# Kernel optimization log

Hardware: AMD Instinct MI355X
Metric: run time of the kernel (lower is better)

## Reference

```python
import jax, jax.numpy as jnp
import numpy as np

NUM_HEADS = 32
NUM_KV_HEADS = 8
HEAD_DIM = 128
ATTN_SCALE = 0.08838834764831845  # 1/sqrt(128)
CONTEXT_LEN = 8192
BLOCK_SIZE = 16
NUM_BLOCKS = 1024  # physical blocks -> 16384 cache slots


def setup_inputs() -> dict:
    key = jax.random.key(0)
    ks = jax.random.split(key, 6)
    q = jax.random.normal(ks[0], (1, NUM_HEADS, HEAD_DIM), jnp.float32)
    k = jax.random.normal(ks[1], (1, NUM_KV_HEADS, HEAD_DIM), jnp.float32)
    v = jax.random.normal(ks[2], (1, NUM_KV_HEADS, HEAD_DIM), jnp.float32)
    num_slots = NUM_BLOCKS * BLOCK_SIZE
    k_cache = jax.random.normal(ks[3], (num_slots, NUM_KV_HEADS, HEAD_DIM), jnp.float32)
    v_cache = jax.random.normal(ks[4], (num_slots, NUM_KV_HEADS, HEAD_DIM), jnp.float32)
    num_logical = CONTEXT_LEN // BLOCK_SIZE
    block_table = jax.random.permutation(ks[5], NUM_BLOCKS)[:num_logical].astype(jnp.int32)
    # new token is written at logical position context_len - 1
    last = CONTEXT_LEN - 1
    slot_mapping = (block_table[last // BLOCK_SIZE] * BLOCK_SIZE + last % BLOCK_SIZE)[None].astype(jnp.int32)
    return {"q": q, "k": k, "v": v, "k_cache": k_cache, "v_cache": v_cache,
            "block_table": block_table, "slot_mapping": slot_mapping,
            "context_len": CONTEXT_LEN, "block_size": BLOCK_SIZE}


def reference(q, k, v, k_cache, v_cache, block_table, slot_mapping, context_len, block_size):
    # _write_to_cache: scatter the new token's K/V into the paged cache
    k_cache = k_cache.at[slot_mapping].set(k)
    v_cache = v_cache.at[slot_mapping].set(v)
    # _build_full_slot_mapping + _read_from_cache: gather full context K/V
    pos = jnp.arange(context_len)
    slots = block_table[pos // block_size] * block_size + pos % block_size  # (S,)
    k_all = k_cache[slots]  # (S, Hkv, D)
    v_all = v_cache[slots]
    # GQA: repeat_interleave KV heads to match query heads
    g = NUM_HEADS // NUM_KV_HEADS
    k_all = jnp.repeat(k_all, g, axis=1)  # (S, H, D)
    v_all = jnp.repeat(v_all, g, axis=1)
    # manual masked SDPA; num_query_tokens == 1 -> mask is all-ones (no tril)
    scores = jnp.einsum('qhd,khd->hqk', q, k_all) * ATTN_SCALE  # (H, 1, S)
    weights = jax.nn.softmax(scores, axis=-1)
    out = jnp.einsum('hqk,khd->qhd', weights, v_all)  # (1, H, D)
    return out
```

## Files before the change

kernel.cpp:

```cpp
#include <hip/hip_runtime.h>
#include <math.h>


#define NUM_HEADS    32
#define NUM_KV_HEADS 8
#define GQA          4
#define HEAD_DIM     128
#define ATTN_SCALE   0.08838834764831845f
#define CTX          8192
#define BLK          16
#define SPLITS       64
#define CHUNK        (CTX / SPLITS)
#define POS_PER_WAVE (CHUNK / 4)
#define ITERS        (POS_PER_WAVE / 2)

__global__ __launch_bounds__(256) void attn_partial(
    const float* __restrict__ q,
    const float* __restrict__ knew,
    const float* __restrict__ vnew,
    const float* __restrict__ kc,
    const float* __restrict__ vc,
    const int*   __restrict__ bt,
    float*       __restrict__ o_part,
    float2*      __restrict__ ml_part)
{
    const int split = blockIdx.x;
    const int kvh   = blockIdx.y;
    const int tid   = threadIdx.x;
    const int wave  = tid >> 6;
    const int lane  = tid & 63;
    const int half  = lane >> 5;
    const int l     = lane & 31;

    float4 qf[GQA];
#pragma unroll
    for (int h = 0; h < GQA; ++h)
        qf[h] = *(const float4*)(q + (kvh * GQA + h) * HEAD_DIM + l * 4);

    float  m[GQA], lsum[GQA];
    float4 o[GQA];
#pragma unroll
    for (int h = 0; h < GQA; ++h) {
        m[h] = -INFINITY; lsum[h] = 0.f;
        o[h] = make_float4(0.f, 0.f, 0.f, 0.f);
    }

    const int base = split * CHUNK + wave * POS_PER_WAVE;

    for (int it = 0; it < ITERS; ++it) {
        const int pos  = base + it * 2 + half;
        const int slot = bt[pos >> 4] * BLK + (pos & 15);

        const float* kptr;
        const float* vptr;
        if (pos == CTX - 1) {
            kptr = knew + kvh * HEAD_DIM;
            vptr = vnew + kvh * HEAD_DIM;
        } else {
            const size_t row = ((size_t)slot * NUM_KV_HEADS + kvh) * HEAD_DIM;
            kptr = kc + row;
            vptr = vc + row;
        }
        const float4 kf = *(const float4*)(kptr + l * 4);
        const float4 vf = *(const float4*)(vptr + l * 4);

        float s[GQA];
#pragma unroll
        for (int h = 0; h < GQA; ++h)
            s[h] = qf[h].x * kf.x + qf[h].y * kf.y + qf[h].z * kf.z + qf[h].w * kf.w;

#pragma unroll
        for (int off = 16; off >= 1; off >>= 1) {
#pragma unroll
            for (int h = 0; h < GQA; ++h)
                s[h] += __shfl_xor(s[h], off, 64);
        }

#pragma unroll
        for (int h = 0; h < GQA; ++h) {
            const float sc    = s[h] * ATTN_SCALE;
            const float mn    = fmaxf(m[h], sc);
            const float alpha = __expf(m[h] - mn);
            const float p     = __expf(sc - mn);
            m[h] = mn;
            lsum[h] = lsum[h] * alpha + p;
            o[h].x = o[h].x * alpha + p * vf.x;
            o[h].y = o[h].y * alpha + p * vf.y;
            o[h].z = o[h].z * alpha + p * vf.z;
            o[h].w = o[h].w * alpha + p * vf.w;
        }
    }

    __shared__ float lds_o[8][GQA][HEAD_DIM];
    __shared__ float lds_m[8][GQA];
    __shared__ float lds_l[8][GQA];

    const int halfid = tid >> 5;
#pragma unroll
    for (int h = 0; h < GQA; ++h) {
        *(float4*)&lds_o[halfid][h][l * 4] = o[h];
        if (l == 0) { lds_m[halfid][h] = m[h]; lds_l[halfid][h] = lsum[h]; }
    }
    __syncthreads();

    if (tid < HEAD_DIM) {
        const int d = tid;
#pragma unroll
        for (int h = 0; h < GQA; ++h) {
            float M = -INFINITY;
#pragma unroll
            for (int i = 0; i < 8; ++i) M = fmaxf(M, lds_m[i][h]);
            float acc = 0.f, L = 0.f;
#pragma unroll
            for (int i = 0; i < 8; ++i) {
                const float w = __expf(lds_m[i][h] - M);
                L   += w * lds_l[i][h];
                acc += w * lds_o[i][h][d];
            }
            const int head = kvh * GQA + h;
            o_part[((size_t)head * SPLITS + split) * HEAD_DIM + d] = acc;
            if (d == 0) ml_part[head * SPLITS + split] = make_float2(M, L);
        }
    }
}

__global__ __launch_bounds__(128) void attn_reduce(
    const float*  __restrict__ o_part,
    const float2* __restrict__ ml_part,
    float*        __restrict__ out)
{
    const int h = blockIdx.x;
    const int d = threadIdx.x;

    __shared__ float2 mls[SPLITS];
    if (d < SPLITS) mls[d] = ml_part[h * SPLITS + d];
    __syncthreads();

    float M = -INFINITY;
#pragma unroll 8
    for (int s = 0; s < SPLITS; ++s) M = fmaxf(M, mls[s].x);

    float acc = 0.f, L = 0.f;
#pragma unroll 4
    for (int s = 0; s < SPLITS; ++s) {
        const float w = __expf(mls[s].x - M);
        L   += w * mls[s].y;
        acc += w * o_part[((size_t)h * SPLITS + s) * HEAD_DIM + d];
    }
    out[h * HEAD_DIM + d] = acc / L;
}

extern "C" void kernel_launch(void* const* d_in, const int* in_sizes, int n_in,
                              void* d_out, int out_size, void* d_ws, size_t ws_size,
                              hipStream_t stream) {
    const float* q    = (const float*)d_in[0];
    const float* knew = (const float*)d_in[1];
    const float* vnew = (const float*)d_in[2];
    const float* kc   = (const float*)d_in[3];
    const float* vc   = (const float*)d_in[4];
    const int*   bt   = (const int*)d_in[5];

    float*  o_part  = (float*)d_ws;
    float2* ml_part = (float2*)((char*)d_ws + (size_t)NUM_HEADS * SPLITS * HEAD_DIM * sizeof(float));

    attn_partial<<<dim3(SPLITS, NUM_KV_HEADS), 256, 0, stream>>>(
        q, knew, vnew, kc, vc, bt, o_part, ml_part);
    attn_reduce<<<NUM_HEADS, HEAD_DIM, 0, stream>>>(o_part, ml_part, (float*)d_out);
}
```

Baseline: 173.4 us.

## Raise split count and batch all KV loads per thread before compute

Raises the number of context splits from 64 to 256, so each block covers 32 positions (two cache blocks) and each half-wave handles 4 positions. All K/V loads for those positions are issued up front into registers, and the two block-table entries are loaded once per block instead of once per position. The goal is more memory-level parallelism and more blocks in flight for this bandwidth-bound decode attention. In exchange, the reduce kernel has to combine 4x more partials and the partial-output workspace traffic grows.

Result: no change. 174.6 us (+0.7%).

```diff
diff --git a/kernel.cpp b/kernel.cpp
--- a/kernel.cpp
+++ b/kernel.cpp
@@ -9,12 +9,11 @@
 #define ATTN_SCALE   0.08838834764831845f
 #define CTX          8192
 #define BLK          16
-#define SPLITS       64
+#define SPLITS       256
 #define CHUNK        (CTX / SPLITS)
-#define POS_PER_WAVE (CHUNK / 4)
-#define ITERS        (POS_PER_WAVE / 2)
+#define PPH          4
 
-__global__ __launch_bounds__(256) void attn_partial(
+__global__ __launch_bounds__(256, 4) void attn_partial(
     const float* __restrict__ q,
     const float* __restrict__ knew,
     const float* __restrict__ vnew,
@@ -32,25 +31,22 @@
     const int half  = lane >> 5;
     const int l     = lane & 31;
 
+    const int bt0 = bt[split * 2];
+    const int bt1 = bt[split * 2 + 1];
+
     float4 qf[GQA];
 #pragma unroll
     for (int h = 0; h < GQA; ++h)
         qf[h] = *(const float4*)(q + (kvh * GQA + h) * HEAD_DIM + l * 4);
 
-    float  m[GQA], lsum[GQA];
-    float4 o[GQA];
+    const int pbase = wave * (2 * PPH) + half;
+    float4 kf[PPH], vf[PPH];
 #pragma unroll
-    for (int h = 0; h < GQA; ++h) {
-        m[h] = -INFINITY; lsum[h] = 0.f;
-        o[h] = make_float4(0.f, 0.f, 0.f, 0.f);
-    }
-
-    const int base = split * CHUNK + wave * POS_PER_WAVE;
-
-    for (int it = 0; it < ITERS; ++it) {
-        const int pos  = base + it * 2 + half;
-        const int slot = bt[pos >> 4] * BLK + (pos & 15);
-
+    for (int it = 0; it < PPH; ++it) {
+        const int off = pbase + it * 2;
+        const int pos = split * CHUNK + off;
+        const int blk = (off >> 4) ? bt1 : bt0;
+        const int slot = blk * BLK + (pos & 15);
         const float* kptr;
         const float* vptr;
         if (pos == CTX - 1) {
@@ -61,33 +57,47 @@
             kptr = kc + row;
             vptr = vc + row;
         }
-        const float4 kf = *(const float4*)(kptr + l * 4);
-        const float4 vf = *(const float4*)(vptr + l * 4);
+        kf[it] = *(const float4*)(kptr + l * 4);
+        vf[it] = *(const float4*)(vptr + l * 4);
+    }
 
-        float s[GQA];
+    float s[PPH][GQA];
+#pragma unroll
+    for (int it = 0; it < PPH; ++it)
 #pragma unroll
         for (int h = 0; h < GQA; ++h)
-            s[h] = qf[h].x * kf.x + qf[h].y * kf.y + qf[h].z * kf.z + qf[h].w * kf.w;
+            s[it][h] = qf[h].x * kf[it].x + qf[h].y * kf[it].y +
+                       qf[h].z * kf[it].z + qf[h].w * kf[it].w;
 
 #pragma unroll
-        for (int off = 16; off >= 1; off >>= 1) {
+    for (int off = 16; off >= 1; off >>= 1)
+#pragma unroll
+        for (int it = 0; it < PPH; ++it)
 #pragma unroll
             for (int h = 0; h < GQA; ++h)
-                s[h] += __shfl_xor(s[h], off, 64);
-        }
+                s[it][h] += __shfl_xor(s[it][h], off, 64);
 
+    float  m[GQA], lsum[GQA];
+    float4 o[GQA];
+#pragma unroll
+    for (int h = 0; h < GQA; ++h) {
+        m[h] = -INFINITY; lsum[h] = 0.f;
+        o[h] = make_float4(0.f, 0.f, 0.f, 0.f);
+    }
+#pragma unroll
+    for (int it = 0; it < PPH; ++it) {
 #pragma unroll
         for (int h = 0; h < GQA; ++h) {
-            const float sc    = s[h] * ATTN_SCALE;
+            const float sc    = s[it][h] * ATTN_SCALE;
             const float mn    = fmaxf(m[h], sc);
             const float alpha = __expf(m[h] - mn);
             const float p     = __expf(sc - mn);
             m[h] = mn;
             lsum[h] = lsum[h] * alpha + p;
-            o[h].x = o[h].x * alpha + p * vf.x;
-            o[h].y = o[h].y * alpha + p * vf.y;
-            o[h].z = o[h].z * alpha + p * vf.z;
-            o[h].w = o[h].w * alpha + p * vf.w;
+            o[h].x = o[h].x * alpha + p * vf[it].x;
+            o[h].y = o[h].y * alpha + p * vf[it].y;
+            o[h].z = o[h].z * alpha + p * vf[it].z;
+            o[h].w = o[h].w * alpha + p * vf[it].w;
         }
     }
 
@@ -133,7 +143,7 @@
     const int d = threadIdx.x;
 
     __shared__ float2 mls[SPLITS];
-    if (d < SPLITS) mls[d] = ml_part[h * SPLITS + d];
+    for (int s = d; s < SPLITS; s += 128) mls[s] = ml_part[h * SPLITS + s];
     __syncthreads();
 
     float M = -INFINITY;
@@ -141,7 +151,7 @@
     for (int s = 0; s < SPLITS; ++s) M = fmaxf(M, mls[s].x);
 
     float acc = 0.f, L = 0.f;
-#pragma unroll 4
+#pragma unroll 8
     for (int s = 0; s < SPLITS; ++s) {
         const float w = __expf(mls[s].x - M);
         L   += w * mls[s].y;
```
